# Performance work log

Hardware: AMD Instinct MI355X
Metric: run time of the kernel (lower is better)

The kernel has to match this reference:

```python
import jax, jax.numpy as jnp
import numpy as np

N_HEAD = 16
N_EMBD = 1024
D_HEAD = N_EMBD // N_HEAD


def setup_inputs() -> dict:
    key = jax.random.key(0)
    ks = jax.random.split(key, 5)
    B, T, C = 4, 2048, N_EMBD
    s = 1.0 / np.sqrt(C)
    return {
        "x": jax.random.normal(ks[0], (B, T, C), dtype=jnp.float32),
        "w_qkv": jax.random.normal(ks[1], (C, 3 * C), dtype=jnp.float32) * s,
        "b_qkv": jnp.zeros((3 * C,), dtype=jnp.float32),
        "w_out": jax.random.normal(ks[2], (C, C), dtype=jnp.float32) * s,
        "b_out": jnp.zeros((C,), dtype=jnp.float32),
    }


def reference(x, w_qkv, b_qkv, w_out, b_out):
    B, T, C = x.shape
    qkv = x @ w_qkv + b_qkv  # [B,T,3C]
    q, k, v = jnp.split(qkv, 3, axis=-1)
    # [B,T,C] -> [B,H,T,D]
    def heads(t):
        return t.reshape(B, T, N_HEAD, D_HEAD).transpose(0, 2, 1, 3)
    q, k, v = heads(q), heads(k), heads(v)
    scores = jnp.einsum("bhqd,bhkd->bhqk", q, k) / np.sqrt(D_HEAD)
    causal = jnp.tril(jnp.ones((T, T), dtype=bool))
    scores = jnp.where(causal, scores, -jnp.inf)
    probs = jax.nn.softmax(scores, axis=-1)
    out = jnp.einsum("bhqk,bhkd->bhqd", probs, v)  # [B,H,T,D]
    out = out.transpose(0, 2, 1, 3).reshape(B, T, C)
    return out @ w_out + b_out
```

## Files before the change

### kernel.cpp

```cpp
#include <hip/hip_runtime.h>
#include <hip/hip_bf16.h>
#include <cstdint>
#include <cstddef>

typedef __attribute__((ext_vector_type(8))) short short8;
typedef __attribute__((ext_vector_type(4))) float f32x4;
typedef __attribute__((ext_vector_type(4))) uint16_t ushort4_t;

__device__ __forceinline__ uint16_t f2bf(float f) {
  union { float f; uint32_t u; } v; v.f = f;
  uint32_t r = v.u + 0x7FFFu + ((v.u >> 16) & 1u);
  return (uint16_t)(r >> 16);
}

__device__ __forceinline__ uint16_t f2bf_hw(float f) {
  union { __hip_bfloat16 h; uint16_t u; } cv;
  cv.h = __float2bfloat16(f);
  return cv.u;
}

__device__ __forceinline__ float fast_exp2(float x) {
#if __has_builtin(__builtin_amdgcn_exp2f)
  return __builtin_amdgcn_exp2f(x);
#else
  return exp2f(x);
#endif
}


__global__ __launch_bounds__(256) void cvt_f32_bf16(const float* __restrict__ in,
                                                    uint16_t* __restrict__ out, int n4) {
  int i = blockIdx.x * 256 + threadIdx.x;
  int stride = gridDim.x * 256;
  for (; i < n4; i += stride) {
    float4 v = ((const float4*)in)[i];
    ushort4_t o = { f2bf(v.x), f2bf(v.y), f2bf(v.z), f2bf(v.w) };
    ((ushort4_t*)out)[i] = o;
  }
}

__global__ __launch_bounds__(256) void transpose_cvt(const float* __restrict__ in,
                                                     uint16_t* __restrict__ out, int R, int C) {
  __shared__ float tile[32][33];
  int c0 = blockIdx.x * 32, r0 = blockIdx.y * 32;
  int tx = threadIdx.x, ty = threadIdx.y;
#pragma unroll
  for (int j = 0; j < 32; j += 8)
    tile[ty + j][tx] = in[(size_t)(r0 + ty + j) * C + c0 + tx];
  __syncthreads();
#pragma unroll
  for (int j = 0; j < 32; j += 8)
    out[(size_t)(c0 + ty + j) * R + r0 + tx] = f2bf(tile[tx][ty + j]);
}

__device__ __forceinline__ void stage16(const uint16_t* g, uint16_t* lds) {
  __builtin_amdgcn_global_load_lds((__attribute__((address_space(1))) void*)g,
                                   (__attribute__((address_space(3))) void*)lds, 16, 0, 0);
}

__global__ __launch_bounds__(256, 3) void gemm_qkv(
    const uint16_t* __restrict__ A, const uint16_t* __restrict__ Bt,
    const float* __restrict__ bias,
    uint16_t* __restrict__ q_out, uint16_t* __restrict__ k_out, uint16_t* __restrict__ vt_out) {
  constexpr int K = 1024, KT = 16;
  __shared__ uint16_t lA[256 * 64];
  __shared__ uint16_t lB[128 * 64];
  const int tid = threadIdx.x;
  const int lane = tid & 63, w = tid >> 6;
  const int wm = w >> 1, wn = w & 1;
  const int r16 = lane & 15, hi = lane >> 4;
  const int wg = (blockIdx.x & 7) * 96 + (blockIdx.x >> 3);
  const int bm = wg / 24, bn = wg % 24;

  const int row0 = tid >> 3;
  const int cch0 = (tid & 7) ^ (row0 & 7);
  const uint16_t* aS = A + ((size_t)bm * 256 + row0) * K + cch0 * 8;
  const uint16_t* bS = Bt + ((size_t)bn * 128 + row0) * K + cch0 * 8;

  f32x4 acc[8][4];
#pragma unroll
  for (int m = 0; m < 8; ++m)
#pragma unroll
    for (int n = 0; n < 4; ++n) acc[m][n] = (f32x4){0.f, 0.f, 0.f, 0.f};

#pragma unroll 1
  for (int kt = 0; kt < KT; ++kt) {
#pragma unroll
    for (int it = 0; it < 8; ++it)
      stage16(aS + (size_t)(it * 32) * K + kt * 64, &lA[it * 2048 + tid * 8]);
#pragma unroll
    for (int it = 0; it < 4; ++it)
      stage16(bS + (size_t)(it * 32) * K + kt * 64, &lB[it * 2048 + tid * 8]);
    __syncthreads();

#pragma unroll
    for (int kk = 0; kk < 2; ++kk) {
      short8 bfr[4];
      const int swz = (kk * 64 + hi * 16) ^ ((r16 & 7) << 4);
#pragma unroll
      for (int n = 0; n < 4; ++n) {
        int rowb = wn * 64 + n * 16 + r16;
        bfr[n] = *(const short8*)((const char*)lB + rowb * 128 + swz);
      }
#pragma unroll
      for (int mh = 0; mh < 2; ++mh) {
        short8 af[4];
#pragma unroll
        for (int i = 0; i < 4; ++i) {
          int rowa = wm * 128 + mh * 64 + i * 16 + r16;
          af[i] = *(const short8*)((const char*)lA + rowa * 128 + swz);
        }
        __builtin_amdgcn_s_setprio(1);
#pragma unroll
        for (int i = 0; i < 4; ++i)
#pragma unroll
          for (int n = 0; n < 4; ++n)
            acc[mh * 4 + i][n] =
                __builtin_amdgcn_mfma_f32_16x16x32_bf16(af[i], bfr[n], acc[mh * 4 + i][n], 0, 0, 0);
        __builtin_amdgcn_s_setprio(0);
      }
    }
    __syncthreads();
  }

  const float SCQ = 0.18033688011112042f;
#pragma unroll
  for (int m = 0; m < 8; ++m) {
    int rg = bm * 256 + wm * 128 + (m >> 2) * 64 + (m & 3) * 16 + hi * 4;
#pragma unroll
    for (int n = 0; n < 4; ++n) {
      int cg = bn * 128 + wn * 64 + n * 16 + r16;
      float bv = bias[cg];
      int which = cg >> 10, hh = (cg >> 6) & 15, dd = cg & 63;
      if (which == 2) {
        int bb = rg >> 11, tt = rg & 2047;
        ushort4_t v4 = { f2bf(acc[m][n][0] + bv), f2bf(acc[m][n][1] + bv),
                         f2bf(acc[m][n][2] + bv), f2bf(acc[m][n][3] + bv) };
        *(ushort4_t*)&vt_out[((size_t)(bb * 16 + hh) * 64 + dd) * 2048 + tt] = v4;
      } else {
        uint16_t* dst = which == 0 ? q_out : k_out;
        float s = which == 0 ? SCQ : 1.0f;
#pragma unroll
        for (int r = 0; r < 4; ++r) {
          int rgr = rg + r;
          dst[((size_t)((rgr >> 11) * 16 + hh) * 2048 + (rgr & 2047)) * 64 + dd] =
              f2bf((acc[m][n][r] + bv) * s);
        }
      }
    }
  }
}


__global__ __launch_bounds__(256) void gemm128_out(
    const uint16_t* __restrict__ A, const uint16_t* __restrict__ Bt,
    const float* __restrict__ bias, int K, float* __restrict__ f_out, int N) {
  __shared__ uint16_t lA[128 * 64];
  __shared__ uint16_t lB[128 * 64];
  const int tid = threadIdx.x;
  const int lane = tid & 63;
  const int w = tid >> 6, wm = w >> 1, wn = w & 1;
  const int r16 = lane & 15, hi = lane >> 4;
  const int bn = blockIdx.x, bm = blockIdx.y;

  f32x4 acc[4][4];
#pragma unroll
  for (int i = 0; i < 4; ++i)
#pragma unroll
    for (int j = 0; j < 4; ++j) acc[i][j] = (f32x4){0.f, 0.f, 0.f, 0.f};

  const int ksteps = K >> 6;
  for (int kt = 0; kt < ksteps; ++kt) {
#pragma unroll
    for (int it = 0; it < 4; ++it) {
      int ci = it * 256 + tid;
      int row = ci >> 3;
      int cch = (ci & 7) ^ (row & 7);
      stage16(A + (size_t)(bm * 128 + row) * K + kt * 64 + cch * 8, &lA[ci * 8]);
      stage16(Bt + (size_t)(bn * 128 + row) * K + kt * 64 + cch * 8, &lB[ci * 8]);
    }
    __syncthreads();
#pragma unroll
    for (int kk = 0; kk < 2; ++kk) {
      short8 af[4], bfr[4];
      int swz = (kk * 64 + hi * 16) ^ ((r16 & 7) << 4);
#pragma unroll
      for (int i = 0; i < 4; ++i) {
        int rowa = wm * 64 + i * 16 + r16;
        af[i] = *(const short8*)((const char*)lA + rowa * 128 + swz);
        int rowb = wn * 64 + i * 16 + r16;
        bfr[i] = *(const short8*)((const char*)lB + rowb * 128 + swz);
      }
#pragma unroll
      for (int i = 0; i < 4; ++i)
#pragma unroll
        for (int j = 0; j < 4; ++j)
          acc[i][j] = __builtin_amdgcn_mfma_f32_16x16x32_bf16(af[i], bfr[j], acc[i][j], 0, 0, 0);
    }
    __syncthreads();
  }

#pragma unroll
  for (int i = 0; i < 4; ++i) {
    int rbase = bm * 128 + wm * 64 + i * 16 + hi * 4;
#pragma unroll
    for (int j = 0; j < 4; ++j) {
      int cg = bn * 128 + wn * 64 + j * 16 + r16;
      float bv = bias[cg];
#pragma unroll
      for (int r = 0; r < 4; ++r)
        f_out[(size_t)(rbase + r) * N + cg] = acc[i][j][r] + bv;
    }
  }
}

__global__ __launch_bounds__(256, 3) void attn_fwd(
    const uint16_t* __restrict__ Qm, const uint16_t* __restrict__ Km,
    const uint16_t* __restrict__ Vt, uint16_t* __restrict__ O) {
  __shared__ uint16_t kbuf[2][64 * 64];
  __shared__ uint16_t vbuf[2][64 * 64];
  __shared__ uint16_t plds[4][32 * 72];
  const int tid = threadIdx.x;
  const int lane = tid & 63, w = tid >> 6;
  const int r16 = lane & 15, hi = lane >> 4;
  const int bid = blockIdx.x;
  const int bh = (bid & 7) + 8 * ((bid >> 3) & 7);
  const int qb = 15 - (bid >> 6);
  const int b = bh >> 4, h = bh & 15;
  const size_t base = (size_t)bh * 2048 * 64;
  const int qlo = qb * 128 + w * 32;
  const int NT = 2 * qb + 2;

  const float BIAS = -20.197730572445487f;

  short8 ones8;
#pragma unroll
  for (int i = 0; i < 8; ++i) ones8[i] = (short)0x3F80;

  short8 aq[2][2];
#pragma unroll
  for (int st = 0; st < 2; ++st)
#pragma unroll
    for (int c = 0; c < 2; ++c)
      aq[st][c] = *(const short8*)&Qm[base + (size_t)(qlo + st * 16 + r16) * 64 + c * 32 + hi * 8];

  f32x4 o[2][4];
  f32x4 o4[2];
#pragma unroll
  for (int st = 0; st < 2; ++st) {
#pragma unroll
    for (int j = 0; j < 4; ++j) o[st][j] = (f32x4){0.f, 0.f, 0.f, 0.f};
    o4[st] = (f32x4){0.f, 0.f, 0.f, 0.f};
  }

  auto stage_tile = [&](int pb, int kv0) {
    {
      int c = tid;            int row = c >> 3, cch = (c & 7) ^ (row & 7);
      stage16(Km + base + (size_t)(kv0 + row) * 64 + cch * 8, &kbuf[pb][c * 8]);
    }
    {
      int c = tid + 256;      int row = c >> 3, cch = (c & 7) ^ (row & 7);
      stage16(Km + base + (size_t)(kv0 + row) * 64 + cch * 8, &kbuf[pb][c * 8]);
    }
    {
      int c = tid;            int row = c >> 3, cch = (c & 7) ^ (row & 7);
      stage16(Vt + base + (size_t)row * 2048 + kv0 + cch * 8, &vbuf[pb][c * 8]);
    }
    {
      int c = tid + 256;      int row = c >> 3, cch = (c & 7) ^ (row & 7);
      stage16(Vt + base + (size_t)row * 2048 + kv0 + cch * 8, &vbuf[pb][c * 8]);
    }
  };

  int pb = 0;
  stage_tile(0, 0);
#pragma unroll 1
  for (int t = 0; t < NT; ++t) {
    const int kv0 = t << 6;
    if (t + 1 < NT) {
      stage_tile(pb ^ 1, (t + 1) << 6);
      asm volatile("s_waitcnt vmcnt(4)" ::: "memory");
    } else {
      asm volatile("s_waitcnt vmcnt(0)" ::: "memory");
    }
    __builtin_amdgcn_s_barrier();
    __builtin_amdgcn_sched_barrier(0);

    if (kv0 <= qlo + 31) {
      const bool maskt = (kv0 + 64 > qlo);
      short8 bk[4][2];
#pragma unroll
      for (int ct = 0; ct < 4; ++ct)
#pragma unroll
        for (int c = 0; c < 2; ++c) {
          int row = ct * 16 + r16;
          int ch = (c * 4 + hi) ^ (row & 7);
          bk[ct][c] = *(const short8*)((const char*)&kbuf[pb][0] + row * 128 + ch * 16);
        }

#pragma unroll
      for (int st = 0; st < 2; ++st) {
        f32x4 sc[4];
#pragma unroll
        for (int ct = 0; ct < 4; ++ct) sc[ct] = (f32x4){BIAS, BIAS, BIAS, BIAS};
        __builtin_amdgcn_s_setprio(1);
#pragma unroll
        for (int ct = 0; ct < 4; ++ct)
#pragma unroll
          for (int c = 0; c < 2; ++c)
            sc[ct] = __builtin_amdgcn_mfma_f32_16x16x32_bf16(bk[ct][c], aq[st][c], sc[ct], 0, 0, 0);
        __builtin_amdgcn_s_setprio(0);

        uint16_t* pl = &plds[w][st * 16 * 72];
        const int qg = qlo + st * 16 + r16;
#pragma unroll
        for (int ct = 0; ct < 4; ++ct) {
          const int kb_ = kv0 + ct * 16 + hi * 4;
          float p0 = fast_exp2(sc[ct][0]);
          float p1 = fast_exp2(sc[ct][1]);
          float p2 = fast_exp2(sc[ct][2]);
          float p3 = fast_exp2(sc[ct][3]);
          if (maskt) {
            if (kb_ + 0 > qg) p0 = 0.f;
            if (kb_ + 1 > qg) p1 = 0.f;
            if (kb_ + 2 > qg) p2 = 0.f;
            if (kb_ + 3 > qg) p3 = 0.f;
          }
          ushort4_t pk4 = { f2bf_hw(p0), f2bf_hw(p1), f2bf_hw(p2), f2bf_hw(p3) };
          *(ushort4_t*)&pl[r16 * 72 + ct * 16 + hi * 4] = pk4;
        }
      }
      asm volatile("s_waitcnt lgkmcnt(0)" ::: "memory");
      __builtin_amdgcn_sched_barrier(0);

      short8 ap[2][2];
#pragma unroll
      for (int st = 0; st < 2; ++st)
#pragma unroll
        for (int ks = 0; ks < 2; ++ks)
          ap[st][ks] = *(const short8*)&plds[w][(st * 16 + r16) * 72 + ks * 32 + hi * 8];
      short8 bv[4][2];
#pragma unroll
      for (int j = 0; j < 4; ++j)
#pragma unroll
        for (int ks = 0; ks < 2; ++ks) {
          int row = j * 16 + r16;
          int ch = (ks * 4 + hi) ^ (row & 7);
          bv[j][ks] = *(const short8*)((const char*)&vbuf[pb][0] + row * 128 + ch * 16);
        }
      __builtin_amdgcn_s_setprio(1);
#pragma unroll
      for (int st = 0; st < 2; ++st) {
#pragma unroll
        for (int ks = 0; ks < 2; ++ks)
          o4[st] = __builtin_amdgcn_mfma_f32_16x16x32_bf16(ones8, ap[st][ks], o4[st], 0, 0, 0);
#pragma unroll
        for (int j = 0; j < 4; ++j)
#pragma unroll
          for (int ks = 0; ks < 2; ++ks)
            o[st][j] = __builtin_amdgcn_mfma_f32_16x16x32_bf16(bv[j][ks], ap[st][ks], o[st][j], 0, 0, 0);
      }
      __builtin_amdgcn_s_setprio(0);
    }

    __builtin_amdgcn_s_barrier();
    __builtin_amdgcn_sched_barrier(0);
    pb ^= 1;
  }

#pragma unroll
  for (int st = 0; st < 2; ++st) {
    float inv = 1.f / o4[st][0];
    int qg = qlo + st * 16 + r16;
    size_t rowo = ((size_t)(b * 2048 + qg)) * 1024 + h * 64;
#pragma unroll
    for (int j = 0; j < 4; ++j) {
      ushort4_t v4 = { f2bf(o[st][j][0] * inv), f2bf(o[st][j][1] * inv),
                       f2bf(o[st][j][2] * inv), f2bf(o[st][j][3] * inv) };
      *(ushort4_t*)&O[rowo + j * 16 + hi * 4] = v4;
    }
  }
}


extern "C" void kernel_launch(void* const* d_in, const int* in_sizes, int n_in,
                              void* d_out, int out_size, void* d_ws, size_t ws_size,
                              hipStream_t stream) {
  const float* x = (const float*)d_in[0];
  const float* w_qkv = (const float*)d_in[1];
  const float* b_qkv = (const float*)d_in[2];
  const float* w_out = (const float*)d_in[3];
  const float* b_out = (const float*)d_in[4];
  float* out = (float*)d_out;

  const size_t BT = 8192, C = 1024, N3 = 3072, BHTD = 8388608;
  char* p = (char*)d_ws;
  uint16_t* xbf = (uint16_t*)p;   p += BT * C * 2;
  uint16_t* wqkvT = (uint16_t*)p; p += N3 * C * 2;
  uint16_t* woutT = (uint16_t*)p; p += C * C * 2;
  uint16_t* qb = (uint16_t*)p;    p += BHTD * 2;
  uint16_t* kb = (uint16_t*)p;    p += BHTD * 2;
  uint16_t* vtb = (uint16_t*)p;   p += BHTD * 2;
  uint16_t* ob = (uint16_t*)p;    p += BHTD * 2;

  cvt_f32_bf16<<<2048, 256, 0, stream>>>(x, xbf, (int)(BT * C / 4));
  transpose_cvt<<<dim3(96, 32), dim3(32, 8), 0, stream>>>(w_qkv, wqkvT, 1024, 3072);
  transpose_cvt<<<dim3(32, 32), dim3(32, 8), 0, stream>>>(w_out, woutT, 1024, 1024);
  gemm_qkv<<<768, 256, 0, stream>>>(xbf, wqkvT, b_qkv, qb, kb, vtb);
  attn_fwd<<<1024, 256, 0, stream>>>(qb, kb, vtb, ob);
  gemm128_out<<<dim3(8, 64), 256, 0, stream>>>(ob, woutT, b_out, 1024, out, 1024);
}
```

Before: 162.6 us.

## Load V tiles directly from global into registers instead of via LDS

Stops staging V^T tiles through shared memory and has each wave read its V fragments straight from global memory, issued after the QK^T MFMAs so the load latency can overlap the softmax work. All QK^T MFMAs for both sub-tiles are also grouped ahead of the exp/mask stage. This cuts LDS footprint, which may allow higher occupancy, and removes LDS write/read traffic for V. In exchange, four waves now fetch the same V data redundantly from global/L2, and the vmcnt accounting changes, so the inline s_waitcnt values may no longer match the outstanding loads.

Result: slower. 192.4 us (+18.3%).

```diff
diff --git a/kernel.cpp b/kernel.cpp
--- a/kernel.cpp
+++ b/kernel.cpp
@@ -218,7 +218,6 @@
     const uint16_t* __restrict__ Qm, const uint16_t* __restrict__ Km,
     const uint16_t* __restrict__ Vt, uint16_t* __restrict__ O) {
   __shared__ uint16_t kbuf[2][64 * 64];
-  __shared__ uint16_t vbuf[2][64 * 64];
   __shared__ uint16_t plds[4][32 * 72];
   const int tid = threadIdx.x;
   const int lane = tid & 63, w = tid >> 6;
@@ -262,14 +261,6 @@
       int c = tid + 256;      int row = c >> 3, cch = (c & 7) ^ (row & 7);
       stage16(Km + base + (size_t)(kv0 + row) * 64 + cch * 8, &kbuf[pb][c * 8]);
     }
-    {
-      int c = tid;            int row = c >> 3, cch = (c & 7) ^ (row & 7);
-      stage16(Vt + base + (size_t)row * 2048 + kv0 + cch * 8, &vbuf[pb][c * 8]);
-    }
-    {
-      int c = tid + 256;      int row = c >> 3, cch = (c & 7) ^ (row & 7);
-      stage16(Vt + base + (size_t)row * 2048 + kv0 + cch * 8, &vbuf[pb][c * 8]);
-    }
   };
 
   int pb = 0;
@@ -279,7 +270,7 @@
     const int kv0 = t << 6;
     if (t + 1 < NT) {
       stage_tile(pb ^ 1, (t + 1) << 6);
-      asm volatile("s_waitcnt vmcnt(4)" ::: "memory");
+      asm volatile("s_waitcnt vmcnt(2)" ::: "memory");
     } else {
       asm volatile("s_waitcnt vmcnt(0)" ::: "memory");
     }
@@ -298,28 +289,39 @@
           bk[ct][c] = *(const short8*)((const char*)&kbuf[pb][0] + row * 128 + ch * 16);
         }
 
+      f32x4 sc[2][4];
+#pragma unroll
+      for (int st = 0; st < 2; ++st)
+#pragma unroll
+        for (int ct = 0; ct < 4; ++ct) sc[st][ct] = (f32x4){BIAS, BIAS, BIAS, BIAS};
+      __builtin_amdgcn_s_setprio(1);
+#pragma unroll
+      for (int st = 0; st < 2; ++st)
+#pragma unroll
+        for (int ct = 0; ct < 4; ++ct)
+#pragma unroll
+          for (int c = 0; c < 2; ++c)
+            sc[st][ct] = __builtin_amdgcn_mfma_f32_16x16x32_bf16(bk[ct][c], aq[st][c], sc[st][ct], 0, 0, 0);
+      __builtin_amdgcn_s_setprio(0);
+
+      short8 bv[4][2];
+#pragma unroll
+      for (int j = 0; j < 4; ++j)
+#pragma unroll
+        for (int ks = 0; ks < 2; ++ks)
+          bv[j][ks] = *(const short8*)&Vt[base + (size_t)(j * 16 + r16) * 2048 + kv0 + ks * 32 + hi * 8];
+
 #pragma unroll
       for (int st = 0; st < 2; ++st) {
-        f32x4 sc[4];
-#pragma unroll
-        for (int ct = 0; ct < 4; ++ct) sc[ct] = (f32x4){BIAS, BIAS, BIAS, BIAS};
-        __builtin_amdgcn_s_setprio(1);
-#pragma unroll
-        for (int ct = 0; ct < 4; ++ct)
-#pragma unroll
-          for (int c = 0; c < 2; ++c)
-            sc[ct] = __builtin_amdgcn_mfma_f32_16x16x32_bf16(bk[ct][c], aq[st][c], sc[ct], 0, 0, 0);
-        __builtin_amdgcn_s_setprio(0);
-
         uint16_t* pl = &plds[w][st * 16 * 72];
         const int qg = qlo + st * 16 + r16;
 #pragma unroll
         for (int ct = 0; ct < 4; ++ct) {
           const int kb_ = kv0 + ct * 16 + hi * 4;
-          float p0 = fast_exp2(sc[ct][0]);
-          float p1 = fast_exp2(sc[ct][1]);
-          float p2 = fast_exp2(sc[ct][2]);
-          float p3 = fast_exp2(sc[ct][3]);
+          float p0 = fast_exp2(sc[st][ct][0]);
+          float p1 = fast_exp2(sc[st][ct][1]);
+          float p2 = fast_exp2(sc[st][ct][2]);
+          float p3 = fast_exp2(sc[st][ct][3]);
           if (maskt) {
             if (kb_ + 0 > qg) p0 = 0.f;
             if (kb_ + 1 > qg) p1 = 0.f;
@@ -339,15 +341,6 @@
 #pragma unroll
         for (int ks = 0; ks < 2; ++ks)
           ap[st][ks] = *(const short8*)&plds[w][(st * 16 + r16) * 72 + ks * 32 + hi * 8];
-      short8 bv[4][2];
-#pragma unroll
-      for (int j = 0; j < 4; ++j)
-#pragma unroll
-        for (int ks = 0; ks < 2; ++ks) {
-          int row = j * 16 + r16;
-          int ch = (ks * 4 + hi) ^ (row & 7);
-          bv[j][ks] = *(const short8*)((const char*)&vbuf[pb][0] + row * 128 + ch * 16);
-        }
       __builtin_amdgcn_s_setprio(1);
 #pragma unroll
       for (int st = 0; st < 2; ++st) {
```
